# Kernel optimization log

Hardware: AMD Instinct MI355X
Metric: run time of the kernel (lower is better)

## Reference

```python
import jax, jax.numpy as jnp
import numpy as np
from jax import lax

PS = 4  # patchsize

def conv2d(x, w, b, pad, dil=1):
    y = lax.conv_general_dilated(x, w, (1, 1), [(pad, pad), (pad, pad)],
                                 rhs_dilation=(dil, dil),
                                 dimension_numbers=('NCHW', 'OIHW', 'NCHW'))
    return y + b[None, :, None, None]

def instance_norm(x, eps=1e-5):
    mu = x.mean(axis=(2, 3), keepdims=True)
    var = x.var(axis=(2, 3), keepdims=True)
    return (x - mu) / jnp.sqrt(var + eps)

def lrelu(x):
    return jnp.where(x >= 0, x, 0.2 * x)

def setup_inputs() -> dict:
    key = jax.random.key(0)
    ks = jax.random.split(key, 20)
    B, C, H, W = 16, 256, 64, 64
    nh, nw = H // PS, W // PS
    N = nh * nw
    s = 0.05
    return {
        'x': jax.random.normal(ks[0], (B, C, H, W), jnp.float32),
        'mask': jax.random.uniform(ks[1], (B, 1, H, W), jnp.float32),
        'dis': jax.random.normal(ks[2], (N, N), jnp.float32),
        'lap_a': jnp.ones((1,), jnp.float32),
        'Wq': jax.random.normal(ks[3], (C, C, 1, 1), jnp.float32) * s,
        'bq': jax.random.normal(ks[4], (C,), jnp.float32) * s,
        'Wk': jax.random.normal(ks[5], (C, C, 1, 1), jnp.float32) * s,
        'bk': jax.random.normal(ks[6], (C,), jnp.float32) * s,
        'Wv': jax.random.normal(ks[7], (C, C, 1, 1), jnp.float32) * s,
        'bv': jax.random.normal(ks[8], (C,), jnp.float32) * s,
        'noise_q': jax.random.normal(ks[9], (B, C, nh, PS, nw, PS), jnp.float32),
        'noise_k': jax.random.normal(ks[10], (B, C, nh, PS, nw, PS), jnp.float32),
        'noise_v': jax.random.normal(ks[11], (B, C, nh, PS, nw, PS), jnp.float32),
        'W_out': jax.random.normal(ks[12], (C, C, 3, 3), jnp.float32) * s,
        'b_out': jax.random.normal(ks[13], (C,), jnp.float32) * s,
        'W1': jax.random.normal(ks[14], (C, C, 3, 3), jnp.float32) * s,
        'b1': jax.random.normal(ks[15], (C,), jnp.float32) * s,
        'W2': jax.random.normal(ks[16], (C, C, 3, 3), jnp.float32) * s,
        'b2': jax.random.normal(ks[17], (C,), jnp.float32) * s,
    }

def _patchify(t, noise, B, C, nh, nw):
    # (B,C,H,W) -> (B,C,nh,PS,nw,PS) + noise -> (B, nh*nw, C*PS*PS)
    t = t.reshape(B, C, nh, PS, nw, PS) + noise
    t = t.transpose(0, 2, 4, 1, 3, 5).reshape(B, nh * nw, C * PS * PS)
    return t

def reference(x, mask, dis, lap_a, Wq, bq, Wk, bk, Wv, bv,
              noise_q, noise_k, noise_v, W_out, b_out, W1, b1, W2, b2):
    B, C, H, W = x.shape
    nh, nw = H // PS, W // PS
    N = nh * nw
    head = PS * 4
    Cp = C * PS * PS
    d = Cp // head

    residual = x
    q = _patchify(conv2d(x, Wq, bq, 0), noise_q, B, C, nh, nw)
    k = _patchify(conv2d(x, Wk, bk, 0), noise_k, B, C, nh, nw)
    v = _patchify(conv2d(x, Wv, bv, 0), noise_v, B, C, nh, nw)

    dis_b = jax.nn.softplus(lap_a)[0] * dis  # (N, N)

    qh = q.reshape(B, N, head, d)
    kh = k.reshape(B, N, head, d)
    vh = v.reshape(B, N, head, d)

    # scores: (head, B, N, N); bias added BEFORE scaling, as in the original
    scores = jnp.einsum('bnhd,bmhd->hbnm', qh, kh)
    scores = (scores + dis_b) / jnp.sqrt(jnp.asarray(d, scores.dtype))

    # mask: patch mean < 0.5 masks key positions
    m = mask.reshape(B, 1, nh, PS, nw, PS).transpose(0, 2, 4, 1, 3, 5)
    m = m.reshape(B, N, PS * PS).mean(-1) < 0.5  # (B, N) bool
    m = jnp.broadcast_to(m[:, None, :], (B, N, N))  # (B, N, N)
    scores = jnp.where(m[None], -jnp.inf, scores)

    p = jax.nn.softmax(scores, axis=-1)
    out = jnp.einsum('hbnm,bmhd->bnhd', p, vh).reshape(B, N, Cp)

    # un-patchify: (B,N,Cp) -> (B,nh,nw,C,PS,PS) -> (B,C,H,W)
    out = out.reshape(B, nh, nw, C, PS, PS).transpose(0, 3, 1, 4, 2, 5).reshape(B, C, H, W)
    out = lrelu(conv2d(out, W_out, b_out, 1)) + residual

    # feed-forward: conv(dil=2) -> IN -> lrelu -> conv -> IN -> lrelu, residual
    y = lrelu(instance_norm(conv2d(out, W1, b1, 2, dil=2)))
    y = lrelu(instance_norm(conv2d(y, W2, b2, 1)))
    return out + y
```

## Files before the change

kernel.cpp:

```cpp
#include <hip/hip_runtime.h>
#include <cstdint>
#include <cstddef>

typedef _Float16 f16;
typedef _Float16 f16x8 __attribute__((ext_vector_type(8)));
typedef _Float16 f16x4 __attribute__((ext_vector_type(4)));
typedef float    f32x4 __attribute__((ext_vector_type(4)));

#define MFMA16(a,b,c) __builtin_amdgcn_mfma_f32_16x16x32_f16((a),(b),(c),0,0,0)

__device__ __forceinline__ float lrelu(float v){ return v >= 0.f ? v : 0.2f*v; }

__device__ __forceinline__ void async_copy16(const f16* g, f16* l){
  __builtin_amdgcn_global_load_lds(
      (const __attribute__((address_space(1))) void*)(uintptr_t)(const void*)g,
      (__attribute__((address_space(3))) void*)(uint32_t)(uintptr_t)(void*)l,
      16, 0, 0);
}


__global__ __launch_bounds__(256) void k_prep1x1(
    const float* __restrict__ wq, const float* __restrict__ wk, const float* __restrict__ wv,
    f16* __restrict__ oq, f16* __restrict__ ok, f16* __restrict__ ov)
{
  int i = blockIdx.x*256 + threadIdx.x;
  int sel = i >> 16, r = i & 65535;
  const float* s = sel==0 ? wq : (sel==1 ? wk : wv);
  f16* d = sel==0 ? oq : (sel==1 ? ok : ov);
  d[r] = (f16)s[r];
}

__global__ __launch_bounds__(256) void k_prep3x3(
    const float* __restrict__ w0, const float* __restrict__ w1, const float* __restrict__ w2,
    f16* __restrict__ o0, f16* __restrict__ o1, f16* __restrict__ o2)
{
  int i = blockIdx.x*256 + threadIdx.x;
  int sel = i / 589824;
  int r = i - sel*589824;
  int t = r >> 16; int rr = r & 65535; int co = rr >> 8; int ci = rr & 255;
  const float* s = sel==0 ? w0 : (sel==1 ? w1 : w2);
  f16* d = sel==0 ? o0 : (sel==1 ? o1 : o2);
  d[r] = (f16)s[(co*256 + ci)*9 + t];
}

__global__ __launch_bounds__(256) void k_pmask(const float* __restrict__ mask, float* __restrict__ pm)
{
  int t = blockIdx.x*256 + threadIdx.x;
  int b = t >> 8, n = t & 255;
  int y0 = (n>>4)<<2, x0 = (n&15)<<2;
  const float* mb = mask + b*4096;
  float s = 0.f;
  #pragma unroll
  for (int i=0;i<4;++i)
    #pragma unroll
    for (int j=0;j<4;++j) s += mb[(y0+i)*64 + x0+j];
  pm[t] = (s*(1.f/16.f) < 0.5f) ? 1.f : 0.f;
}

__global__ __launch_bounds__(256) void k_nchw2nhwc(
    const float* __restrict__ src, const float2* __restrict__ st, f16* __restrict__ dst)
{
  int idx = blockIdx.x;
  int y = idx & 63, b = idx >> 6;
  int tid = threadIdx.x;
  __shared__ f16 T[64*264];

  {
    const float* row = src + (size_t)(b*256+tid)*4096 + y*64;
    float mu = 0.f, ri = 1.f;
    bool doin = (st != nullptr);
    if (doin){ float2 s = st[b*256+tid]; mu = s.x; ri = s.y; }
    #pragma unroll
    for (int j=0;j<16;++j){
      float4 u = *(const float4*)(row + j*4);
      int x = j*4;
      float a0=(u.x-mu)*ri, a1=(u.y-mu)*ri, a2=(u.z-mu)*ri, a3=(u.w-mu)*ri;
      if (doin){ a0=lrelu(a0); a1=lrelu(a1); a2=lrelu(a2); a3=lrelu(a3); }
      T[(x+0)*264+tid]=(f16)a0; T[(x+1)*264+tid]=(f16)a1;
      T[(x+2)*264+tid]=(f16)a2; T[(x+3)*264+tid]=(f16)a3;
    }
  }
  __syncthreads();
  {
    int oct = tid & 31, pxl = tid >> 5;
    #pragma unroll
    for (int p=0;p<8;++p){
      int px = p*8 + pxl;
      *(uint4*)&dst[((size_t)((b*64+y)*64+px)<<8) + oct*8] = *(const uint4*)&T[px*264 + oct*8];
    }
  }
}

__global__ __launch_bounds__(256, 4) void k_qkv(
    const f16* __restrict__ xh,
    const f16* __restrict__ wq, const f16* __restrict__ wk, const f16* __restrict__ wv,
    const float* __restrict__ bq, const float* __restrict__ bk, const float* __restrict__ bv,
    const float* __restrict__ nq, const float* __restrict__ nk, const float* __restrict__ nv,
    f16* __restrict__ Qp, f16* __restrict__ Kp, f16* __restrict__ Vt)
{
  int idx = blockIdx.x;
  int yt  = idx & 15; idx >>= 4;
  int cot = idx & 3;  idx >>= 2;
  int b   = idx & 15; idx >>= 4;
  int sel = idx;
  int tid = threadIdx.x;
  int wave = tid>>6, lane = tid&63, quad = lane>>4, l16 = lane&15;
  int co0 = cot*64, y0 = yt*4;

  const f16*  W    = sel==0 ? wq : (sel==1 ? wk : wv);
  const float* bias= sel==0 ? bq : (sel==1 ? bk : bv);
  const float* nz  = sel==0 ? nq : (sel==1 ? nk : nv);

  __shared__ f16 smem[20480];

  f32x4 acc[16];
  #pragma unroll
  for (int i=0;i<16;++i){ acc[i][0]=0.f; acc[i][1]=0.f; acc[i][2]=0.f; acc[i][3]=0.f; }

  int g8 = (((lane&3) ^ ((lane>>3)&3)) << 3);
  const f16* Wrow = W + ((co0 + wave*16 + (lane>>2))<<8) + g8;
  const f16* Xrow = xh + (((size_t)((b*64 + y0)*64))<<8) + g8;

  auto stage = [&](int buf, int kc){
    int ci0 = kc<<5;
    f16* Ab = smem + buf*2048;
    f16* Bb = smem + 4096 + buf*8192;
    async_copy16(Wrow + ci0, Ab + wave*512);
    #pragma unroll
    for (int j=0;j<4;++j){
      int px = j*64 + wave*16 + (lane>>2);
      async_copy16(Xrow + ((size_t)px<<8) + ci0, Bb + (j*64 + wave*16)*32);
    }
  };

  stage(0, 0);
  #pragma unroll
  for (int kc=0; kc<8; ++kc){
    int cur = kc & 1;
    if (kc < 7){
      stage(cur^1, kc+1);
      asm volatile("s_waitcnt vmcnt(5)\n\ts_barrier" ::: "memory");
    } else {
      asm volatile("s_waitcnt vmcnt(0)\n\ts_barrier" ::: "memory");
    }
    const f16* Al = smem + cur*2048;
    const f16* Bl = smem + 4096 + cur*8192;
    f16x8 af = *(const f16x8*)&Al[(wave*16+l16)*32 + ((quad ^ ((l16>>1)&3))<<3)];
    #pragma unroll
    for (int nt=0;nt<16;++nt){
      int bidx = (nt>>2)*64 + (nt&3)*16 + l16;
      f16x8 bf = *(const f16x8*)&Bl[bidx*32 + ((quad ^ ((bidx>>1)&3))<<3)];
      acc[nt] = MFMA16(af, bf, acc[nt]);
    }
    asm volatile("s_waitcnt lgkmcnt(0)\n\ts_barrier" ::: "memory");
  }

  int cob = co0 + wave*16 + quad*4;
  int h0 = cot*4, pr = yt;
  float bs[4];
  #pragma unroll
  for (int r=0;r<4;++r) bs[r] = bias[cob+r];

  const float* nzb = nz + ((size_t)(b*256 + co0) << 12) + y0*64;

  #pragma unroll
  for (int half=0; half<2; ++half){
    #pragma unroll
    for (int p=0;p<8;++p){
      int i = p*256 + tid;
      int c32 = i>>6, px0 = (i&63)*4;
      float4 u = *(const float4*)(nzb + (((size_t)(half*32 + c32))<<12) + px0);
      f16x4 h4; h4[0]=(f16)u.x; h4[1]=(f16)u.y; h4[2]=(f16)u.z; h4[3]=(f16)u.w;
      *(f16x4*)&smem[c32*256 + (px0 ^ (((c32>>2)&3)<<4))] = h4;
    }
    __syncthreads();
    if ((wave>>1) == half){
      #pragma unroll
      for (int nt=0;nt<16;++nt){
        int px = (nt>>2)*64 + (nt&3)*16 + l16;
        int n_ = (nt&3)*4 + (l16>>2);
        int ddb = (quad<<6) + ((nt>>2)<<2) + (l16&3);
        #pragma unroll
        for (int r=0;r<4;++r){
          int c32 = ((wave&1)<<4) + (quad<<2) + r;
          float nzv = (float)smem[c32*256 + (px ^ (((c32>>2)&3)<<4))];
          float v = acc[nt][r] + bs[r] + nzv;
          int dd = ddb + (r<<4);
          if (sel < 2){
            int row = ((wave&1)<<4) + n_;
            smem[8192 + row*280 + dd + ((dd>>6)<<3)] = (f16)v;
          } else {
            smem[8192 + ((wave&1)*4128) + dd*16 + ((dd>>6)<<3) + n_] = (f16)v;
          }
        }
      }
    }
    __syncthreads();
    if (sel < 2){
      f16* dst = sel==0 ? Qp : Kp;
      #pragma unroll
      for (int pass=0; pass<4; ++pass){
        int rowi = pass*8 + (tid>>5);
        int ch  = tid & 31;
        uint4 v = *(const uint4*)&smem[8192 + rowi*280 + ch*8 + ((ch>>3)<<3)];
        int grow = half*32 + rowi;
        *(uint4*)&dst[((b*16 + h0 + (grow>>4))<<16) + ((pr*16 + (grow&15))<<8) + ch*8] = v;
      }
    } else {
      #pragma unroll
      for (int p=0;p<4;++p){
        int i = p*256 + tid;
        int rw = i>>1, hf = i&1;
        int dd = rw & 255;
        uint4 v = *(const uint4*)&smem[8192 + (rw>>8)*4128 + dd*16 + ((dd>>6)<<3) + hf*8];
        *(uint4*)&Vt[((b*16 + h0 + half*2 + (rw>>8))<<16) + (dd<<8) + pr*16 + hf*8] = v;
      }
    }
    __syncthreads();
  }
}

__global__ __launch_bounds__(256) void k_attn(
    const f16* __restrict__ Qp, const f16* __restrict__ Kp, const f16* __restrict__ Vt,
    const float* __restrict__ dis, const float* __restrict__ lap_a,
    const float* __restrict__ pm, f16* __restrict__ attn)
{
  int idx = blockIdx.x;
  int nt = idx & 3; idx >>= 2;
  int h  = idx & 15; idx >>= 4;
  int b  = idx;
  int tid = threadIdx.x, wave = tid>>6, lane = tid&63, quad = lane>>4, l16 = lane&15;
  int n0 = nt*64;
  int bh = (b*16 + h) << 16;

  __shared__ f16 smem[25344];
  f16* Ql  = smem;
  f16* KVl = smem + 16896;

  {
    int row = tid>>2, part = (tid&3)*64;
    const uint4* s = (const uint4*)&Qp[bh + ((n0+row)<<8) + part];
    uint4* d = (uint4*)&Ql[row*264 + part];
    #pragma unroll
    for (int j=0;j<8;++j) d[j] = s[j];
  }

  float splus = log1pf(expf(lap_a[0]));

  f32x4 sacc[16];
  #pragma unroll
  for (int i=0;i<16;++i){ sacc[i][0]=0.f; sacc[i][1]=0.f; sacc[i][2]=0.f; sacc[i][3]=0.f; }

  #pragma unroll
  for (int mc=0; mc<8; ++mc){
    __syncthreads();
    {
      int row = tid>>3, part = (tid&7)*32;
      const uint4* s = (const uint4*)&Kp[bh + ((mc*32+row)<<8) + part];
      uint4* d = (uint4*)&KVl[row*264 + part];
      #pragma unroll
      for (int j=0;j<4;++j) d[j] = s[j];
    }
    __syncthreads();
    #pragma unroll
    for (int kk=0;kk<8;++kk){
      f16x8 af = *(const f16x8*)&Ql[(wave*16+l16)*264 + kk*32 + quad*8];
      #pragma unroll
      for (int j=0;j<2;++j){
        f16x8 bf = *(const f16x8*)&KVl[(j*16+l16)*264 + kk*32 + quad*8];
        sacc[mc*2+j] = MFMA16(af, bf, sacc[mc*2+j]);
      }
    }
  }

  int nrow_base = wave*16 + quad*4;
  float pmv[16];
  #pragma unroll
  for (int t=0;t<16;++t) pmv[t] = pm[b*256 + t*16 + l16];

  #pragma unroll
  for (int r=0;r<4;++r){
    int n = n0 + nrow_base + r;
    float sv[16];
    float mx = -1e30f;
    #pragma unroll
    for (int t=0;t<16;++t){
      float s = sacc[t][r];
      s = (s + splus * dis[n*256 + t*16 + l16]) * 0.0625f;
      s = (pmv[t] > 0.5f) ? -1e30f : s;
      sv[t] = s;
      mx = fmaxf(mx, s);
    }
    #pragma unroll
    for (int off=1; off<16; off<<=1) mx = fmaxf(mx, __shfl_xor(mx, off, 64));
    float sum = 0.f;
    #pragma unroll
    for (int t=0;t<16;++t){ float e = __expf(sv[t]-mx); sv[t]=e; sum += e; }
    #pragma unroll
    for (int off=1; off<16; off<<=1) sum += __shfl_xor(sum, off, 64);
    float inv = 1.f/sum;
    #pragma unroll
    for (int t=0;t<16;++t) Ql[(nrow_base + r)*264 + t*16 + l16] = (f16)(sv[t]*inv);
  }

  f32x4 oacc[16];
  #pragma unroll
  for (int i=0;i<16;++i){ oacc[i][0]=0.f; oacc[i][1]=0.f; oacc[i][2]=0.f; oacc[i][3]=0.f; }

  for (int dc=0; dc<8; ++dc){
    __syncthreads();
    {
      int row = tid>>3, part = (tid&7)*32;
      const uint4* s = (const uint4*)&Vt[bh + ((dc*32+row)<<8) + part];
      uint4* d = (uint4*)&KVl[row*264 + part];
      #pragma unroll
      for (int j=0;j<4;++j) d[j] = s[j];
    }
    __syncthreads();
    #pragma unroll
    for (int kk=0;kk<8;++kk){
      f16x8 af = *(const f16x8*)&Ql[(wave*16+l16)*264 + kk*32 + quad*8];
      #pragma unroll
      for (int j=0;j<2;++j){
        f16x8 bf = *(const f16x8*)&KVl[(j*16+l16)*264 + kk*32 + quad*8];
        oacc[dc*2+j] = MFMA16(af, bf, oacc[dc*2+j]);
      }
    }
  }

  __syncthreads();
  #pragma unroll
  for (int dc=0; dc<8; ++dc){
    #pragma unroll
    for (int j=0;j<2;++j){
      int dd = dc*32 + j*16 + l16;
      int c_ = dd>>4;
      int pi = (dd>>2)&3, pj = dd&3;
      #pragma unroll
      for (int r=0;r<4;++r){
        int nl = nrow_base + r;
        int y_ = ((nl>>4)<<2) + pi;
        int x  = ((nl&15)<<2) + pj;
        smem[(y_*64 + x)*24 + c_] = (f16)oacc[dc*2+j][r];
      }
    }
  }
  __syncthreads();
  #pragma unroll
  for (int p=0;p<4;++p){
    int pix = p*256 + tid;
    int y_ = pix>>6, x = pix&63;
    uint4 v0 = *(const uint4*)&smem[pix*24];
    uint4 v1 = *(const uint4*)&smem[pix*24 + 8];
    size_t o = ((size_t)((b*64 + nt*16 + y_)*64 + x)<<8) + h*16;
    *(uint4*)&attn[o]     = v0;
    *(uint4*)&attn[o + 8] = v1;
  }
}

template<int DIL, int MODE>
__global__ __launch_bounds__(256) void k_conv3(
    const f16* __restrict__ in, const f16* __restrict__ Wt, const float* __restrict__ bias,
    const float* __restrict__ resid, float* __restrict__ outf, f16* __restrict__ outh)
{
  int idx = blockIdx.x;
  int yt  = idx & 15; idx >>= 4;
  int cot = idx & 3;  idx >>= 2;
  int b   = idx;
  int y0 = yt*4, co0 = cot*64;
  int tid = threadIdx.x;
  int wave = tid>>6, lane = tid&63, quad = lane>>4, l16 = lane&15;

  __shared__ float cs4[8192];
  f16* Al = (f16*)cs4;
  f16* Bl = (f16*)cs4 + 7680;

  f32x4 acc[16];
  #pragma unroll
  for (int i=0;i<16;++i){ acc[i][0]=0.f; acc[i][1]=0.f; acc[i][2]=0.f; acc[i][3]=0.f; }

  constexpr int PXR = 64 + 2*DIL;
  constexpr int NU4 = 16*PXR;

  for (int ky=0; ky<3; ++ky){
    int yb = y0 + DIL*(ky-1);
    for (int kc=0; kc<8; ++kc){
      int ci0 = kc*32;
      {
        int aco = tid>>2, ap = (tid&3)*8;
        #pragma unroll
        for (int kx=0;kx<3;++kx)
          *(uint4*)&Al[kx*2560 + aco*40 + ap] =
              *(const uint4*)&Wt[((ky*3+kx)<<16) + ((co0+aco)<<8) + ci0 + ap];
      }
      #pragma unroll
      for (int p=0;p<5;++p){
        int i = p*256 + tid;
        if (i < NU4){
          int px = i>>2, oct = i&3;
          int yr = px / PXR, xp = px - yr*PXR;
          int yy = yb + yr, xx = xp - DIL;
          uint4 v = make_uint4(0u,0u,0u,0u);
          if (yy>=0 && yy<64 && xx>=0 && xx<64)
            v = *(const uint4*)&in[((size_t)((b*64+yy)*64+xx)<<8) + ci0 + oct*8];
          int si = yr*68 + xp;
          *(uint4*)&Bl[si*32 + ((oct ^ (si&3))<<3)] = v;
        }
      }
      __syncthreads();
      #pragma unroll
      for (int kx=0;kx<3;++kx){
        f16x8 af = *(const f16x8*)&Al[kx*2560 + (wave*16+l16)*40 + quad*8];
        #pragma unroll
        for (int nt=0;nt<16;++nt){
          int bidx = (nt>>2)*68 + (nt&3)*16 + l16 + kx*DIL;
          f16x8 bf = *(const f16x8*)&Bl[bidx*32 + ((quad ^ (bidx&3))<<3)];
          acc[nt] = MFMA16(af, bf, acc[nt]);
        }
      }
      __syncthreads();
    }
  }

  int cob = co0 + wave*16 + quad*4;
  float bs[4];
  #pragma unroll
  for (int r=0;r<4;++r) bs[r] = bias[cob+r];

  if (MODE==0){
    const float* rb = resid + ((size_t)(b*256 + co0) << 12) + y0*64;
    #pragma unroll
    for (int half=0; half<2; ++half){
      #pragma unroll
      for (int p=0;p<8;++p){
        int i = p*256 + tid;
        int c32 = i>>6, px0 = (i&63)*4;
        float4 u = *(const float4*)(rb + (((size_t)(half*32 + c32))<<12) + px0);
        *(float4*)&cs4[c32*256 + (px0 ^ (((c32>>2)&3)<<3))] = u;
      }
      __syncthreads();
      if ((wave>>1) == half){
        #pragma unroll
        for (int nt=0;nt<16;++nt){
          int y = y0 + (nt>>2), x = (nt&3)*16 + l16;
          int px = (nt>>2)*64 + (nt&3)*16 + l16;
          #pragma unroll
          for (int r=0;r<4;++r){
            int co = cob + r;
            int c32 = ((wave&1)<<4) + (quad<<2) + r;
            float rv = cs4[c32*256 + (px ^ (((c32>>2)&3)<<3))];
            float v = lrelu(acc[nt][r] + bs[r]) + rv;
            size_t o = (size_t)(b*256+co)*4096 + y*64 + x;
            outf[o] = v;
            outh[((size_t)((b*64+y)*64+x)<<8) + co] = (f16)v;
          }
        }
      }
      __syncthreads();
    }
  } else {
    #pragma unroll
    for (int nt=0;nt<16;++nt){
      int y = y0 + (nt>>2), x = (nt&3)*16 + l16;
      #pragma unroll
      for (int r=0;r<4;++r){
        int co = cob + r;
        float v = acc[nt][r] + bs[r];
        size_t o = (size_t)(b*256+co)*4096 + y*64 + x;
        outf[o] = v;
      }
    }
  }
}

__global__ __launch_bounds__(256) void k_instats(const float* __restrict__ v, float2* __restrict__ st)
{
  int bc = blockIdx.x;
  const float* p = v + (size_t)bc*4096;
  int tid = threadIdx.x;
  float s=0.f, ss=0.f;
  #pragma unroll
  for (int it=0; it<4; ++it){
    float4 u = *(const float4*)(p + it*1024 + tid*4);
    s  += u.x+u.y+u.z+u.w;
    ss += u.x*u.x + u.y*u.y + u.z*u.z + u.w*u.w;
  }
  #pragma unroll
  for (int off=32; off; off>>=1){ s += __shfl_down(s, off, 64); ss += __shfl_down(ss, off, 64); }
  __shared__ float rs[4], rss[4];
  int wave = tid>>6, lane = tid&63;
  if (lane==0){ rs[wave]=s; rss[wave]=ss; }
  __syncthreads();
  if (tid==0){
    float S = rs[0]+rs[1]+rs[2]+rs[3], SS = rss[0]+rss[1]+rss[2]+rss[3];
    float mu = S*(1.f/4096.f);
    float var = SS*(1.f/4096.f) - mu*mu;
    st[bc] = make_float2(mu, rsqrtf(var + 1e-5f));
  }
}

__global__ __launch_bounds__(256) void k_final(float* __restrict__ out, const float* __restrict__ c2,
                                               const float2* __restrict__ st)
{
  int i4 = blockIdx.x*256 + threadIdx.x;
  float2 s = st[i4>>10];
  float4 u = *(const float4*)(c2 + (size_t)i4*4);
  float4 o = *(const float4*)(out + (size_t)i4*4);
  o.x += lrelu((u.x - s.x)*s.y);
  o.y += lrelu((u.y - s.x)*s.y);
  o.z += lrelu((u.z - s.x)*s.y);
  o.w += lrelu((u.w - s.x)*s.y);
  *(float4*)(out + (size_t)i4*4) = o;
}

extern "C" void kernel_launch(void* const* d_in, const int* in_sizes, int n_in,
                              void* d_out, int out_size, void* d_ws, size_t ws_size,
                              hipStream_t stream)
{
  const float* x    = (const float*)d_in[0];
  const float* mask = (const float*)d_in[1];
  const float* dis  = (const float*)d_in[2];
  const float* lapa = (const float*)d_in[3];
  const float* Wq   = (const float*)d_in[4];
  const float* bq   = (const float*)d_in[5];
  const float* Wk   = (const float*)d_in[6];
  const float* bk   = (const float*)d_in[7];
  const float* Wv   = (const float*)d_in[8];
  const float* bv   = (const float*)d_in[9];
  const float* nq   = (const float*)d_in[10];
  const float* nk   = (const float*)d_in[11];
  const float* nv   = (const float*)d_in[12];
  const float* Wo   = (const float*)d_in[13];
  const float* bo   = (const float*)d_in[14];
  const float* W1   = (const float*)d_in[15];
  const float* b1   = (const float*)d_in[16];
  const float* W2   = (const float*)d_in[17];
  const float* b2   = (const float*)d_in[18];

  char* w = (char*)d_ws;
  f16*   xh    = (f16*)(w + 0);
  f16*   Qp    = (f16*)(w + 33554432);
  f16*   Kp    = (f16*)(w + 67108864);
  f16*   Vt    = (f16*)(w + 100663296);
  f16*   attnb = (f16*)(w + 134217728);
  f16*   outbf = (f16*)(w + 0);
  float* c1    = (float*)(w + 33554432);
  f16*   y1    = (f16*)(w + 100663296);
  float* c2    = (float*)(w + 33554432);
  f16*   wqh   = (f16*)(w + 167772160);
  f16*   wkh   = wqh + 65536;
  f16*   wvh   = wkh + 65536;
  f16*   wt0   = (f16*)(w + 168165376);
  f16*   wt1   = wt0 + 589824;
  f16*   wt2   = wt1 + 589824;
  float* pmk   = (float*)(w + 171704320);
  float2* st1  = (float2*)(w + 171720704);
  float2* st2  = (float2*)(w + 171753472);
  float* out   = (float*)d_out;

  k_prep1x1<<<768, 256, 0, stream>>>(Wq, Wk, Wv, wqh, wkh, wvh);
  k_prep3x3<<<6912, 256, 0, stream>>>(Wo, W1, W2, wt0, wt1, wt2);
  k_pmask<<<16, 256, 0, stream>>>(mask, pmk);
  k_nchw2nhwc<<<1024, 256, 0, stream>>>(x, nullptr, xh);
  k_qkv<<<3072, 256, 0, stream>>>(xh, wqh, wkh, wvh, bq, bk, bv, nq, nk, nv, Qp, Kp, Vt);
  k_attn<<<1024, 256, 0, stream>>>(Qp, Kp, Vt, dis, lapa, pmk, attnb);
  k_conv3<1,0><<<1024, 256, 0, stream>>>(attnb, wt0, bo, x, out, outbf);
  k_conv3<2,1><<<1024, 256, 0, stream>>>(outbf, wt1, b1, nullptr, c1, nullptr);
  k_instats<<<4096, 256, 0, stream>>>(c1, st1);
  k_nchw2nhwc<<<1024, 256, 0, stream>>>(c1, st1, y1);
  k_conv3<1,1><<<1024, 256, 0, stream>>>(y1, wt2, b2, nullptr, c2, nullptr);
  k_instats<<<4096, 256, 0, stream>>>(c2, st2);
  k_final<<<16384, 256, 0, stream>>>(out, c2, st2);
}
```

Baseline: 971.6 us.

## Double-buffer conv3 input tiles with async global-to-LDS copies and register-held weights

The 3x3 conv kernel now stages input tiles straight into LDS with global_load_lds async copies into two buffers, loading the next K-chunk while MFMAs run on the current one. Weight fragments are loaded directly from global into registers and prefetched one step ahead instead of going through LDS. Out-of-bounds pixels read from a zeroed scratch buffer set up by the mask kernel, the LDS swizzle changes to suit the async copy lane layout, and launch bounds ask for 4 blocks per CU. This aims to hide global load latency and halve the barriers per step, at the cost of more registers and 35KB of LDS per block.

```diff
diff --git a/kernel.cpp b/kernel.cpp
--- a/kernel.cpp
+++ b/kernel.cpp
@@ -43,9 +43,11 @@
   d[r] = (f16)s[(co*256 + ci)*9 + t];
 }
 
-__global__ __launch_bounds__(256) void k_pmask(const float* __restrict__ mask, float* __restrict__ pm)
+__global__ __launch_bounds__(256) void k_pmask(const float* __restrict__ mask, float* __restrict__ pm,
+                                               float* __restrict__ zp)
 {
   int t = blockIdx.x*256 + threadIdx.x;
+  if (t < 16) zp[t] = 0.f;
   int b = t >> 8, n = t & 255;
   int y0 = (n>>4)<<2, x0 = (n&15)<<2;
   const float* mb = mask + b*4096;
@@ -359,9 +361,10 @@
 }
 
 template<int DIL, int MODE>
-__global__ __launch_bounds__(256) void k_conv3(
+__global__ __launch_bounds__(256, 4) void k_conv3(
     const f16* __restrict__ in, const f16* __restrict__ Wt, const float* __restrict__ bias,
-    const float* __restrict__ resid, float* __restrict__ outf, f16* __restrict__ outh)
+    const float* __restrict__ resid, float* __restrict__ outf, f16* __restrict__ outh,
+    const float* __restrict__ zp)
 {
   int idx = blockIdx.x;
   int yt  = idx & 15; idx >>= 4;
@@ -371,56 +374,63 @@
   int tid = threadIdx.x;
   int wave = tid>>6, lane = tid&63, quad = lane>>4, l16 = lane&15;
 
-  __shared__ float cs4[8192];
-  f16* Al = (f16*)cs4;
-  f16* Bl = (f16*)cs4 + 7680;
+  __shared__ f16 smem[17920];
 
   f32x4 acc[16];
   #pragma unroll
   for (int i=0;i<16;++i){ acc[i][0]=0.f; acc[i][1]=0.f; acc[i][2]=0.f; acc[i][3]=0.f; }
 
-  constexpr int PXR = 64 + 2*DIL;
-  constexpr int NU4 = 16*PXR;
-
-  for (int ky=0; ky<3; ++ky){
-    int yb = y0 + DIL*(ky-1);
-    for (int kc=0; kc<8; ++kc){
-      int ci0 = kc*32;
-      {
-        int aco = tid>>2, ap = (tid&3)*8;
-        #pragma unroll
-        for (int kx=0;kx<3;++kx)
-          *(uint4*)&Al[kx*2560 + aco*40 + ap] =
-              *(const uint4*)&Wt[((ky*3+kx)<<16) + ((co0+aco)<<8) + ci0 + ap];
-      }
-      #pragma unroll
-      for (int p=0;p<5;++p){
-        int i = p*256 + tid;
-        if (i < NU4){
-          int px = i>>2, oct = i&3;
-          int yr = px / PXR, xp = px - yr*PXR;
-          int yy = yb + yr, xx = xp - DIL;
-          uint4 v = make_uint4(0u,0u,0u,0u);
-          if (yy>=0 && yy<64 && xx>=0 && xx<64)
-            v = *(const uint4*)&in[((size_t)((b*64+yy)*64+xx)<<8) + ci0 + oct*8];
-          int si = yr*68 + xp;
-          *(uint4*)&Bl[si*32 + ((oct ^ (si&3))<<3)] = v;
-        }
-      }
-      __syncthreads();
-      #pragma unroll
-      for (int kx=0;kx<3;++kx){
-        f16x8 af = *(const f16x8*)&Al[kx*2560 + (wave*16+l16)*40 + quad*8];
-        #pragma unroll
-        for (int nt=0;nt<16;++nt){
-          int bidx = (nt>>2)*68 + (nt&3)*16 + l16 + kx*DIL;
-          f16x8 bf = *(const f16x8*)&Bl[bidx*32 + ((quad ^ (bidx&3))<<3)];
-          acc[nt] = MFMA16(af, bf, acc[nt]);
-        }
-      }
-      __syncthreads();
-    }
-  }
+  const f16* zp16 = (const f16*)zp;
+  int oct = (lane&3) ^ ((lane>>3)&3);
+  int rl  = lane>>2;
+  const f16* wbase = Wt + ((co0 + wave*16 + l16)<<8) + quad*8;
+
+  auto stageB = [&](int buf, int ky, int kc){
+    int ci0 = kc<<5;
+    int ybase = y0 + DIL*(ky-1);
+    f16* Bb = smem + buf*8704;
+    #pragma unroll
+    for (int j=0;j<5;++j){
+      int si = j*64 + wave*16 + rl;
+      int yr = si / 68;
+      int xp = si - yr*68;
+      int yy = ybase + yr, xx = xp - DIL;
+      bool valid = (si < 272) && (yy>=0) && (yy<64) && (xx>=0) && (xx<64);
+      const f16* src = valid ? &in[((size_t)((b*64+yy)*64+xx)<<8) + ci0 + oct*8] : zp16;
+      f16* dst = (j==4 && wave!=0) ? (smem + 17408) : (Bb + (j*64 + wave*16)*32);
+      async_copy16(src, dst);
+    }
+  };
+
+  f16x8 afc[3], afn[3];
+  #pragma unroll
+  for (int kx=0;kx<3;++kx){ afc[kx] = *(const f16x8*)&wbase[kx<<16]; afn[kx] = afc[kx]; }
+  stageB(0, 0, 0);
+
+  for (int t=0; t<24; ++t){
+    int cur = t & 1;
+    asm volatile("s_waitcnt vmcnt(0)\n\ts_barrier" ::: "memory");
+    if (t < 23){
+      int tn = t+1, kyn = tn>>3, kcn = tn&7;
+      stageB(cur^1, kyn, kcn);
+      #pragma unroll
+      for (int kx=0;kx<3;++kx)
+        afn[kx] = *(const f16x8*)&wbase[((kyn*3+kx)<<16) + (kcn<<5)];
+    }
+    const f16* Bl = smem + cur*8704;
+    #pragma unroll
+    for (int kx=0;kx<3;++kx){
+      #pragma unroll
+      for (int nt=0;nt<16;++nt){
+        int bidx = (nt>>2)*68 + (nt&3)*16 + l16 + kx*DIL;
+        f16x8 bf = *(const f16x8*)&Bl[bidx*32 + ((quad ^ ((bidx>>1)&3))<<3)];
+        acc[nt] = MFMA16(afc[kx], bf, acc[nt]);
+      }
+    }
+    #pragma unroll
+    for (int kx=0;kx<3;++kx) afc[kx] = afn[kx];
+  }
+  asm volatile("s_waitcnt lgkmcnt(0)\n\ts_barrier" ::: "memory");
 
   int cob = co0 + wave*16 + quad*4;
   float bs[4];
@@ -428,6 +438,7 @@
   for (int r=0;r<4;++r) bs[r] = bias[cob+r];
 
   if (MODE==0){
+    float* cs4 = (float*)smem;
     const float* rb = resid + ((size_t)(b*256 + co0) << 12) + y0*64;
     #pragma unroll
     for (int half=0; half<2; ++half){
@@ -556,19 +567,20 @@
   float* pmk   = (float*)(w + 171704320);
   float2* st1  = (float2*)(w + 171720704);
   float2* st2  = (float2*)(w + 171753472);
+  float* zpk   = (float*)(w + 171786240);
   float* out   = (float*)d_out;
 
   k_prep1x1<<<768, 256, 0, stream>>>(Wq, Wk, Wv, wqh, wkh, wvh);
   k_prep3x3<<<6912, 256, 0, stream>>>(Wo, W1, W2, wt0, wt1, wt2);
-  k_pmask<<<16, 256, 0, stream>>>(mask, pmk);
+  k_pmask<<<16, 256, 0, stream>>>(mask, pmk, zpk);
   k_nchw2nhwc<<<1024, 256, 0, stream>>>(x, nullptr, xh);
   k_qkv<<<3072, 256, 0, stream>>>(xh, wqh, wkh, wvh, bq, bk, bv, nq, nk, nv, Qp, Kp, Vt);
   k_attn<<<1024, 256, 0, stream>>>(Qp, Kp, Vt, dis, lapa, pmk, attnb);
-  k_conv3<1,0><<<1024, 256, 0, stream>>>(attnb, wt0, bo, x, out, outbf);
-  k_conv3<2,1><<<1024, 256, 0, stream>>>(outbf, wt1, b1, nullptr, c1, nullptr);
+  k_conv3<1,0><<<1024, 256, 0, stream>>>(attnb, wt0, bo, x, out, outbf, zpk);
+  k_conv3<2,1><<<1024, 256, 0, stream>>>(outbf, wt1, b1, nullptr, c1, nullptr, zpk);
   k_instats<<<4096, 256, 0, stream>>>(c1, st1);
   k_nchw2nhwc<<<1024, 256, 0, stream>>>(c1, st1, y1);
-  k_conv3<1,1><<<1024, 256, 0, stream>>>(y1, wt2, b2, nullptr, c2, nullptr);
+  k_conv3<1,1><<<1024, 256, 0, stream>>>(y1, wt2, b2, nullptr, c2, nullptr, zpk);
   k_instats<<<4096, 256, 0, stream>>>(c2, st2);
   k_final<<<16384, 256, 0, stream>>>(out, c2, st2);
 }
```

Result: slower. 1.517 ms (+56.1%).
